# Kernel tuning notes

Measured on AMD Instinct MI355X. Metric: run time of the kernel, lower is better.

## Reference

```python
import jax, jax.numpy as jnp
import numpy as np

WIN = (2, 7, 7)  # (H, W, D) window size

def _relative_position_index(H, W, D):
    coords = np.stack(np.meshgrid(np.arange(H), np.arange(W), np.arange(D), indexing='ij'))
    cf = coords.reshape(3, -1)  # [3, N]
    rel = cf[:, :, None] - cf[:, None, :]  # [3, N, N]
    rel = rel.transpose(1, 2, 0).copy()
    rel[:, :, 0] += H - 1
    rel[:, :, 1] += W - 1
    rel[:, :, 2] += D - 1
    rel[:, :, 0] *= (2 * W - 1) * (2 * D - 1)
    rel[:, :, 1] *= 2 * D - 1
    return jnp.asarray(rel.sum(-1), dtype=jnp.int32)  # [N, N]

def setup_inputs() -> dict:
    key = jax.random.key(0)
    ks = jax.random.split(key, 7)
    H, W, D = WIN
    N = H * W * D          # 98
    C = 192
    nh = 6
    num_windows = 64
    B_ = 8 * num_windows   # 512
    x = jax.random.normal(ks[0], (B_, N, C), dtype=jnp.float32)
    # shifted-window attention mask: 0 for allowed pairs, -100 for masked
    mask = jnp.where(jax.random.uniform(ks[1], (num_windows, N, N)) < 0.9, 0.0, -100.0).astype(jnp.float32)
    qkv_w = jax.random.normal(ks[2], (3 * C, C), dtype=jnp.float32) * 0.02
    qkv_b = jnp.zeros((3 * C,), dtype=jnp.float32)
    out_w = jax.random.normal(ks[3], (C, C), dtype=jnp.float32) * 0.02
    out_b = jnp.zeros((C,), dtype=jnp.float32)
    table_len = (2 * H - 1) * (2 * W - 1) * (2 * D - 1)  # 507
    bias_table = jax.random.normal(ks[4], (table_len, nh), dtype=jnp.float32) * 0.02
    rel_index = _relative_position_index(H, W, D)
    return {"x": x, "mask": mask, "qkv_w": qkv_w, "qkv_b": qkv_b,
            "out_w": out_w, "out_b": out_b, "bias_table": bias_table,
            "rel_index": rel_index}

def reference(x, mask, qkv_w, qkv_b, out_w, out_b, bias_table, rel_index):
    B_, N, C = x.shape
    nh = bias_table.shape[1]
    d = C // nh
    scale = d ** (-0.5)
    qkv = (x @ qkv_w.T + qkv_b).reshape(B_, N, 3, nh, d)
    qkv = qkv.transpose(2, 0, 3, 1, 4)          # [3, B_, nh, N, d]
    q, k, v = qkv[0], qkv[1], qkv[2]
    attn = jnp.einsum('bhnd,bhmd->bhnm', q, k) * scale   # [B_, nh, N, N]
    bias = bias_table[rel_index]                 # [N, N, nh]
    attn = attn + bias.transpose(2, 0, 1)[None]  # add relative position bias
    nw = mask.shape[0]
    attn = attn.reshape(B_ // nw, nw, nh, N, N) + mask[None, :, None]
    attn = attn.reshape(B_, nh, N, N)
    p = jax.nn.softmax(attn, axis=-1)
    out = jnp.einsum('bhnm,bhmd->bhnd', p, v)    # [B_, nh, N, d]
    out = out.transpose(0, 2, 1, 3).reshape(B_, N, C)
    return out @ out_w.T + out_b
```

## Files before the change

### kernel.cpp

```cpp
#include <hip/hip_runtime.h>

typedef __attribute__((ext_vector_type(8))) __bf16 bf16x8;
typedef __attribute__((ext_vector_type(4))) float f32x4;
typedef __attribute__((ext_vector_type(8))) unsigned short us8;
typedef __attribute__((ext_vector_type(4))) unsigned short us4;

#define NTOK 98
#define NPAD 112
#define CDIM 192
#define NH 6
#define HD 32
#define NWIN 64
#define BWIN 512
#define MROWS (BWIN * NTOK)
#define QKVN (3 * CDIM)
#define NN (NTOK * NTOK)
#define SCALE 0.17677669529663687f

#define PREP_BIAS (NH * NN)
#define PREP_WQ (QKVN * CDIM)
#define PREP_WO (CDIM * CDIM)
#define PREP_TOT (PREP_BIAS + PREP_WQ + PREP_WO)

__device__ __forceinline__ unsigned short f2b(float f) {
  unsigned u = __builtin_bit_cast(unsigned, f);
  u += 0x7FFFu + ((u >> 16) & 1u);
  return (unsigned short)(u >> 16);
}

__device__ __forceinline__ bf16x8 ldfrag(const unsigned short* p) {
  return __builtin_bit_cast(bf16x8, *(const us8*)p);
}

__global__ __launch_bounds__(256) void k_prep(
    const float* __restrict__ table, const int* __restrict__ relidx,
    const float* __restrict__ wq, const float* __restrict__ wo,
    float* __restrict__ biasHT, unsigned short* __restrict__ wqb,
    unsigned short* __restrict__ wob) {
  int idx = blockIdx.x * 256 + threadIdx.x;
  if (idx < PREP_BIAS) {
    int h = idx / NN, ij = idx - h * NN;
    biasHT[idx] = table[relidx[ij] * NH + h];
    return;
  }
  int i2 = idx - PREP_BIAS;
  if (i2 < PREP_WQ) { if (i2 >= 0) wqb[i2] = f2b(wq[i2]); return; }
  int i3 = i2 - PREP_WQ;
  if (i3 < PREP_WO) wob[i3] = f2b(wo[i3]);
}

__global__ __launch_bounds__(256) void k_qkv(
    const float* __restrict__ x, const unsigned short* __restrict__ wqb,
    const float* __restrict__ bias, unsigned short* __restrict__ qkv) {
  __shared__ unsigned short As[128 * 200];
  __shared__ unsigned short Bs[64 * 200];
  const int tid = threadIdx.x;
  const int m0 = blockIdx.x * 128;
  for (int it = 0; it < 24; ++it) {
    int q = it * 256 + tid;
    int row = q / 48, c4 = q - row * 48;
    float4 v = *(const float4*)(x + (m0 + row) * CDIM + c4 * 4);
    us4 u = {f2b(v.x), f2b(v.y), f2b(v.z), f2b(v.w)};
    *(us4*)&As[row * 200 + c4 * 4] = u;
  }
  const int lane = tid & 63;
  const int l15 = lane & 15, hi = lane >> 4;
  const int wr = (tid >> 6) >> 1, wc = (tid >> 6) & 1;
  __syncthreads();
  for (int j = 0; j < 9; ++j) {
    for (int it = 0; it < 6; ++it) {
      int q = it * 256 + tid;
      int row = q / 24, c8 = q - row * 24;
      *(us8*)&Bs[row * 200 + c8 * 8] = *(const us8*)(wqb + (j * 64 + row) * CDIM + c8 * 8);
    }
    __syncthreads();
    f32x4 acc[4][2];
#pragma unroll
    for (int fr = 0; fr < 4; ++fr) { acc[fr][0] = (f32x4)0.f; acc[fr][1] = (f32x4)0.f; }
#pragma unroll
    for (int ks = 0; ks < 6; ++ks) {
      int k0 = ks * 32 + hi * 8;
      bf16x8 b0 = ldfrag(&Bs[(wc * 32 + l15) * 200 + k0]);
      bf16x8 b1 = ldfrag(&Bs[(wc * 32 + 16 + l15) * 200 + k0]);
#pragma unroll
      for (int fr = 0; fr < 4; ++fr) {
        bf16x8 a = ldfrag(&As[(wr * 64 + fr * 16 + l15) * 200 + k0]);
        acc[fr][0] = __builtin_amdgcn_mfma_f32_16x16x32_bf16(a, b0, acc[fr][0], 0, 0, 0);
        acc[fr][1] = __builtin_amdgcn_mfma_f32_16x16x32_bf16(a, b1, acc[fr][1], 0, 0, 0);
      }
    }
    __syncthreads();
#pragma unroll
    for (int fr = 0; fr < 4; ++fr)
#pragma unroll
      for (int fc = 0; fc < 2; ++fc) {
        int colb = j * 64 + wc * 32 + fc * 16;
        int t = (colb >= 2 * CDIM) ? 2 : (colb >= CDIM ? 1 : 0);
        int head = (colb >> 5) - t * NH;
        int d = (colb & 31) + l15;
        long pbase = ((long)(t * NH + head) * MROWS) * 32 + d;
#pragma unroll
        for (int r = 0; r < 4; ++r) {
          int row = m0 + wr * 64 + fr * 16 + hi * 4 + r;
          float v = acc[fr][fc][r] + bias[colb + l15];
          if (t == 0) v *= SCALE;
          qkv[pbase + (long)row * 32] = f2b(v);
        }
      }
  }
}

__global__ __launch_bounds__(448) void k_attn(
    const unsigned short* __restrict__ qkv, const float* __restrict__ biasHT,
    const float* __restrict__ mask, unsigned short* __restrict__ ao) {
  __shared__ unsigned short Ks[NPAD * 40];
  __shared__ unsigned short Vt[32 * 136];
  __shared__ unsigned short P[NPAD * 136];
  const int tid = threadIdx.x;
  const int h = blockIdx.x % NH;
  const int b = blockIdx.x / NH;
  const int wnd = b & (NWIN - 1);
  const int lane = tid & 63, wv = tid >> 6;
  const int l15 = lane & 15, hi = lane >> 4;
  const long rb = (long)b * NTOK;
  const unsigned short* qp = qkv + ((long)h * MROWS + rb) * 32;
  const unsigned short* kp = qkv + ((long)(NH + h) * MROWS + rb) * 32;
  const unsigned short* vp = qkv + ((long)(2 * NH + h) * MROWS + rb) * 32;
  {
    int row = tid >> 2, q = tid & 3;
    us8 kv = (us8)0;
    if (row < NTOK) kv = *(const us8*)(kp + row * 32 + q * 8);
    *(us8*)&Ks[row * 40 + q * 8] = kv;
    if (row < NTOK) {
      us8 vv = *(const us8*)(vp + row * 32 + q * 8);
#pragma unroll
      for (int i = 0; i < 8; ++i) Vt[(q * 8 + i) * 136 + row] = vv[i];
    }
    for (int i = tid; i < 32 * 38; i += 448) {
      int dd = i / 38, n = NTOK + (i - dd * 38);
      Vt[dd * 136 + n] = 0;
    }
    for (int i = tid; i < NPAD * 16; i += 448)
      P[(i >> 4) * 136 + 112 + (i & 15)] = 0;
  }
  int qn = wv * 16 + l15;
  us8 qu = (us8)0;
  if (qn < NTOK) qu = *(const us8*)(qp + qn * 32 + hi * 8);
  bf16x8 qf = __builtin_bit_cast(bf16x8, qu);
  __syncthreads();
  f32x4 sacc[7];
#pragma unroll
  for (int tc = 0; tc < 7; ++tc) {
    bf16x8 kb = ldfrag(&Ks[(tc * 16 + l15) * 40 + hi * 8]);
    sacc[tc] = __builtin_amdgcn_mfma_f32_16x16x32_bf16(qf, kb, (f32x4)0.f, 0, 0, 0);
  }
  const float* bp = biasHT + h * NN;
  const float* mp = mask + wnd * NN;
  float rsum[4];
#pragma unroll
  for (int r = 0; r < 4; ++r) {
    int row = wv * 16 + hi * 4 + r;
    float sv[7];
    float m = -1e30f;
#pragma unroll
    for (int tc = 0; tc < 7; ++tc) {
      int col = tc * 16 + l15;
      float val = -1e30f;
      if (col < NTOK && row < NTOK) {
        int o = row * NTOK + col;
        val = (sacc[tc][r] + bp[o]) + mp[o];
      }
      sv[tc] = val;
      m = fmaxf(m, val);
    }
#pragma unroll
    for (int off = 1; off < 16; off <<= 1) m = fmaxf(m, __shfl_xor(m, off));
    float s = 0.f;
#pragma unroll
    for (int tc = 0; tc < 7; ++tc) {
      float e = __expf(sv[tc] - m);
      s += e;
      P[row * 136 + tc * 16 + l15] = f2b(e);
    }
#pragma unroll
    for (int off = 1; off < 16; off <<= 1) s += __shfl_xor(s, off);
    rsum[r] = s;
  }
  f32x4 oacc[2];
  oacc[0] = (f32x4)0.f; oacc[1] = (f32x4)0.f;
#pragma unroll
  for (int ks = 0; ks < 4; ++ks) {
    int k0 = ks * 32 + hi * 8;
    bf16x8 pa = ldfrag(&P[(wv * 16 + l15) * 136 + k0]);
#pragma unroll
    for (int tc = 0; tc < 2; ++tc) {
      bf16x8 vb = ldfrag(&Vt[(tc * 16 + l15) * 136 + k0]);
      oacc[tc] = __builtin_amdgcn_mfma_f32_16x16x32_bf16(pa, vb, oacc[tc], 0, 0, 0);
    }
  }
#pragma unroll
  for (int tc = 0; tc < 2; ++tc)
#pragma unroll
    for (int r = 0; r < 4; ++r) {
      int row = wv * 16 + hi * 4 + r;
      if (row < NTOK) {
        float v = oacc[tc][r] / rsum[r];
        ao[(rb + row) * CDIM + h * HD + tc * 16 + l15] = f2b(v);
      }
    }
}

__global__ __launch_bounds__(256) void k_proj(
    const unsigned short* __restrict__ a, const unsigned short* __restrict__ wob,
    const float* __restrict__ bias, float* __restrict__ out) {
  __shared__ unsigned short As[128 * 200];
  __shared__ unsigned short Bs[64 * 200];
  const int tid = threadIdx.x;
  const int m0 = blockIdx.x * 128;
  for (int it = 0; it < 12; ++it) {
    int q = it * 256 + tid;
    int row = q / 24, c8 = q - row * 24;
    *(us8*)&As[row * 200 + c8 * 8] = *(const us8*)(a + (m0 + row) * CDIM + c8 * 8);
  }
  const int lane = tid & 63;
  const int l15 = lane & 15, hi = lane >> 4;
  const int wr = (tid >> 6) >> 1, wc = (tid >> 6) & 1;
  __syncthreads();
  for (int j = 0; j < 3; ++j) {
    for (int it = 0; it < 6; ++it) {
      int q = it * 256 + tid;
      int row = q / 24, c8 = q - row * 24;
      *(us8*)&Bs[row * 200 + c8 * 8] = *(const us8*)(wob + (j * 64 + row) * CDIM + c8 * 8);
    }
    __syncthreads();
    f32x4 acc[4][2];
#pragma unroll
    for (int fr = 0; fr < 4; ++fr) { acc[fr][0] = (f32x4)0.f; acc[fr][1] = (f32x4)0.f; }
#pragma unroll
    for (int ks = 0; ks < 6; ++ks) {
      int k0 = ks * 32 + hi * 8;
      bf16x8 b0 = ldfrag(&Bs[(wc * 32 + l15) * 200 + k0]);
      bf16x8 b1 = ldfrag(&Bs[(wc * 32 + 16 + l15) * 200 + k0]);
#pragma unroll
      for (int fr = 0; fr < 4; ++fr) {
        bf16x8 aa = ldfrag(&As[(wr * 64 + fr * 16 + l15) * 200 + k0]);
        acc[fr][0] = __builtin_amdgcn_mfma_f32_16x16x32_bf16(aa, b0, acc[fr][0], 0, 0, 0);
        acc[fr][1] = __builtin_amdgcn_mfma_f32_16x16x32_bf16(aa, b1, acc[fr][1], 0, 0, 0);
      }
    }
    __syncthreads();
#pragma unroll
    for (int fr = 0; fr < 4; ++fr)
#pragma unroll
      for (int fc = 0; fc < 2; ++fc)
#pragma unroll
        for (int r = 0; r < 4; ++r) {
          int row = m0 + wr * 64 + fr * 16 + hi * 4 + r;
          int col = j * 64 + wc * 32 + fc * 16 + l15;
          out[row * CDIM + col] = acc[fr][fc][r] + bias[col];
        }
  }
}

extern "C" void kernel_launch(void* const* d_in, const int* in_sizes, int n_in,
                              void* d_out, int out_size, void* d_ws, size_t ws_size,
                              hipStream_t stream) {
  const float* x      = (const float*)d_in[0];
  const float* mask   = (const float*)d_in[1];
  const float* qkv_w  = (const float*)d_in[2];
  const float* qkv_b  = (const float*)d_in[3];
  const float* out_w  = (const float*)d_in[4];
  const float* out_b  = (const float*)d_in[5];
  const float* table  = (const float*)d_in[6];
  const int*   relidx = (const int*)d_in[7];
  float* out = (float*)d_out;
  char* ws = (char*)d_ws;

  const size_t off_bias = 0;
  const size_t off_wqb  = 230656;
  const size_t off_wob  = 451840;
  const size_t off_qkv  = 525568;
  const size_t off_ao   = off_qkv + 57802752;
  float* biasHT = (float*)(ws + off_bias);
  unsigned short* wqb  = (unsigned short*)(ws + off_wqb);
  unsigned short* wob  = (unsigned short*)(ws + off_wob);
  unsigned short* qkvp = (unsigned short*)(ws + off_qkv);
  unsigned short* aop  = (unsigned short*)(ws + off_ao);

  k_prep<<<(PREP_TOT + 255) / 256, 256, 0, stream>>>(table, relidx, qkv_w, out_w,
                                                     biasHT, wqb, wob);
  k_qkv<<<MROWS / 128, 256, 0, stream>>>(x, wqb, qkv_b, qkvp);
  k_attn<<<BWIN * NH, 448, 0, stream>>>(qkvp, biasHT, mask, aop);
  k_proj<<<MROWS / 128, 256, 0, stream>>>(aop, wob, out_b, out);
}
```

Baseline: 198.2 us.

## Fuse QKV projection and attention per window, premerge bias and mask

Replaces the separate QKV GEMM and attention kernels with one kernel per window. It computes Q, K and V for all six heads into LDS and then runs attention for each head. This removes the global write and re-read of the full bf16 QKV tensor. The prep kernel now builds one combined relative-position-bias-plus-mask table per window and head, so attention does a single load per score instead of two. The cost is a large LDS footprint that allows only one 448-thread block per CU. The weight tiles are also restaged nine times per block with barriers, and the merged table adds about 15 MB of prep writes per call.

```diff
diff --git a/kernel.cpp b/kernel.cpp
--- a/kernel.cpp
+++ b/kernel.cpp
@@ -6,21 +6,24 @@
 typedef __attribute__((ext_vector_type(4))) unsigned short us4;
 
 #define NTOK 98
-#define NPAD 112
 #define CDIM 192
 #define NH 6
-#define HD 32
 #define NWIN 64
 #define BWIN 512
 #define MROWS (BWIN * NTOK)
-#define QKVN (3 * CDIM)
 #define NN (NTOK * NTOK)
 #define SCALE 0.17677669529663687f
 
-#define PREP_BIAS (NH * NN)
-#define PREP_WQ (QKVN * CDIM)
+#define PREP_BM (NWIN * NH * NN)
+#define PREP_WQ (3 * CDIM * CDIM)
 #define PREP_WO (CDIM * CDIM)
-#define PREP_TOT (PREP_BIAS + PREP_WQ + PREP_WO)
+#define PREP_TOT (PREP_BM + PREP_WQ + PREP_WO)
+
+#define OFF_AS 0
+#define OFF_W  39200
+#define OFF_K  64800
+#define OFF_VT 118560
+#define LDS_TOT 161824
 
 __device__ __forceinline__ unsigned short f2b(float f) {
   unsigned u = __builtin_bit_cast(unsigned, f);
@@ -34,180 +37,197 @@
 
 __global__ __launch_bounds__(256) void k_prep(
     const float* __restrict__ table, const int* __restrict__ relidx,
-    const float* __restrict__ wq, const float* __restrict__ wo,
-    float* __restrict__ biasHT, unsigned short* __restrict__ wqb,
-    unsigned short* __restrict__ wob) {
+    const float* __restrict__ mask, const float* __restrict__ wq,
+    const float* __restrict__ wo, float* __restrict__ bm,
+    unsigned short* __restrict__ wqb, unsigned short* __restrict__ wob) {
   int idx = blockIdx.x * 256 + threadIdx.x;
-  if (idx < PREP_BIAS) {
-    int h = idx / NN, ij = idx - h * NN;
-    biasHT[idx] = table[relidx[ij] * NH + h];
+  if (idx < PREP_BM) {
+    int w = idx / (NH * NN);
+    int r = idx - w * NH * NN;
+    int h = r / NN, ij = r - h * NN;
+    bm[idx] = table[relidx[ij] * NH + h] + mask[w * NN + ij];
     return;
   }
-  int i2 = idx - PREP_BIAS;
-  if (i2 < PREP_WQ) { if (i2 >= 0) wqb[i2] = f2b(wq[i2]); return; }
+  int i2 = idx - PREP_BM;
+  if (i2 < PREP_WQ) { wqb[i2] = f2b(wq[i2]); return; }
   int i3 = i2 - PREP_WQ;
-  if (i3 < PREP_WO) wob[i3] = f2b(wo[i3]);
-}
-
-__global__ __launch_bounds__(256) void k_qkv(
+  if (i3 < PREP_TOT - PREP_BM - PREP_WQ) wob[i3] = f2b(wo[i3]);
+}
+
+__global__ __launch_bounds__(448, 2) void k_fused(
     const float* __restrict__ x, const unsigned short* __restrict__ wqb,
-    const float* __restrict__ bias, unsigned short* __restrict__ qkv) {
-  __shared__ unsigned short As[128 * 200];
-  __shared__ unsigned short Bs[64 * 200];
+    const float* __restrict__ qkv_b, const float* __restrict__ bm,
+    unsigned short* __restrict__ ao) {
+  extern __shared__ char smem[];
+  unsigned short* As = (unsigned short*)(smem + OFF_AS);
+  unsigned short* Ws = (unsigned short*)(smem + OFF_W);
+  unsigned short* Ks = (unsigned short*)(smem + OFF_K);
+  unsigned short* Vt = (unsigned short*)(smem + OFF_VT);
   const int tid = threadIdx.x;
-  const int m0 = blockIdx.x * 128;
-  for (int it = 0; it < 24; ++it) {
-    int q = it * 256 + tid;
-    int row = q / 48, c4 = q - row * 48;
-    float4 v = *(const float4*)(x + (m0 + row) * CDIM + c4 * 4);
-    us4 u = {f2b(v.x), f2b(v.y), f2b(v.z), f2b(v.w)};
-    *(us4*)&As[row * 200 + c4 * 4] = u;
-  }
-  const int lane = tid & 63;
-  const int l15 = lane & 15, hi = lane >> 4;
-  const int wr = (tid >> 6) >> 1, wc = (tid >> 6) & 1;
-  __syncthreads();
-  for (int j = 0; j < 9; ++j) {
-    for (int it = 0; it < 6; ++it) {
-      int q = it * 256 + tid;
-      int row = q / 24, c8 = q - row * 24;
-      *(us8*)&Bs[row * 200 + c8 * 8] = *(const us8*)(wqb + (j * 64 + row) * CDIM + c8 * 8);
-    }
-    __syncthreads();
-    f32x4 acc[4][2];
-#pragma unroll
-    for (int fr = 0; fr < 4; ++fr) { acc[fr][0] = (f32x4)0.f; acc[fr][1] = (f32x4)0.f; }
-#pragma unroll
-    for (int ks = 0; ks < 6; ++ks) {
-      int k0 = ks * 32 + hi * 8;
-      bf16x8 b0 = ldfrag(&Bs[(wc * 32 + l15) * 200 + k0]);
-      bf16x8 b1 = ldfrag(&Bs[(wc * 32 + 16 + l15) * 200 + k0]);
-#pragma unroll
-      for (int fr = 0; fr < 4; ++fr) {
-        bf16x8 a = ldfrag(&As[(wr * 64 + fr * 16 + l15) * 200 + k0]);
-        acc[fr][0] = __builtin_amdgcn_mfma_f32_16x16x32_bf16(a, b0, acc[fr][0], 0, 0, 0);
-        acc[fr][1] = __builtin_amdgcn_mfma_f32_16x16x32_bf16(a, b1, acc[fr][1], 0, 0, 0);
-      }
-    }
-    __syncthreads();
-#pragma unroll
-    for (int fr = 0; fr < 4; ++fr)
-#pragma unroll
-      for (int fc = 0; fc < 2; ++fc) {
-        int colb = j * 64 + wc * 32 + fc * 16;
-        int t = (colb >= 2 * CDIM) ? 2 : (colb >= CDIM ? 1 : 0);
-        int head = (colb >> 5) - t * NH;
-        int d = (colb & 31) + l15;
-        long pbase = ((long)(t * NH + head) * MROWS) * 32 + d;
-#pragma unroll
-        for (int r = 0; r < 4; ++r) {
-          int row = m0 + wr * 64 + fr * 16 + hi * 4 + r;
-          float v = acc[fr][fc][r] + bias[colb + l15];
-          if (t == 0) v *= SCALE;
-          qkv[pbase + (long)row * 32] = f2b(v);
-        }
-      }
-  }
-}
-
-__global__ __launch_bounds__(448) void k_attn(
-    const unsigned short* __restrict__ qkv, const float* __restrict__ biasHT,
-    const float* __restrict__ mask, unsigned short* __restrict__ ao) {
-  __shared__ unsigned short Ks[NPAD * 40];
-  __shared__ unsigned short Vt[32 * 136];
-  __shared__ unsigned short P[NPAD * 136];
-  const int tid = threadIdx.x;
-  const int h = blockIdx.x % NH;
-  const int b = blockIdx.x / NH;
-  const int wnd = b & (NWIN - 1);
+  const int b = blockIdx.x;
   const int lane = tid & 63, wv = tid >> 6;
   const int l15 = lane & 15, hi = lane >> 4;
-  const long rb = (long)b * NTOK;
-  const unsigned short* qp = qkv + ((long)h * MROWS + rb) * 32;
-  const unsigned short* kp = qkv + ((long)(NH + h) * MROWS + rb) * 32;
-  const unsigned short* vp = qkv + ((long)(2 * NH + h) * MROWS + rb) * 32;
-  {
-    int row = tid >> 2, q = tid & 3;
-    us8 kv = (us8)0;
-    if (row < NTOK) kv = *(const us8*)(kp + row * 32 + q * 8);
-    *(us8*)&Ks[row * 40 + q * 8] = kv;
-    if (row < NTOK) {
-      us8 vv = *(const us8*)(vp + row * 32 + q * 8);
-#pragma unroll
-      for (int i = 0; i < 8; ++i) Vt[(q * 8 + i) * 136 + row] = vv[i];
-    }
-    for (int i = tid; i < 32 * 38; i += 448) {
-      int dd = i / 38, n = NTOK + (i - dd * 38);
-      Vt[dd * 136 + n] = 0;
-    }
-    for (int i = tid; i < NPAD * 16; i += 448)
-      P[(i >> 4) * 136 + 112 + (i & 15)] = 0;
-  }
-  int qn = wv * 16 + l15;
-  us8 qu = (us8)0;
-  if (qn < NTOK) qu = *(const us8*)(qp + qn * 32 + hi * 8);
-  bf16x8 qf = __builtin_bit_cast(bf16x8, qu);
+  unsigned short* scr = Ws + wv * 640;
+
+  for (int it = 0; it < 11; ++it) {
+    int q = it * 448 + tid;
+    if (q < 98 * 48) {
+      int row = q / 48, c4 = q - row * 48;
+      float4 v = *(const float4*)(x + ((size_t)b * NTOK + row) * CDIM + c4 * 4);
+      us4 u = {f2b(v.x), f2b(v.y), f2b(v.z), f2b(v.w)};
+      *(us4*)&As[row * 200 + c4 * 4] = u;
+    }
+  }
+
+#define STAGEW(J)                                                              \
+  for (int it = 0; it < 4; ++it) {                                             \
+    int q = it * 448 + tid;                                                    \
+    if (q < 1536) {                                                            \
+      int row = q / 24, c8 = q - row * 24;                                     \
+      *(us8*)&Ws[row * 200 + c8 * 8] =                                         \
+          *(const us8*)(wqb + ((J) * 64 + row) * CDIM + c8 * 8);               \
+    }                                                                          \
+  }
+
+#define DOMFMA(ACC)                                                            \
+  _Pragma("unroll") for (int ks = 0; ks < 6; ++ks) {                           \
+    int k0 = ks * 32 + hi * 8;                                                 \
+    bf16x8 a = ldfrag(&As[(wv * 16 + l15) * 200 + k0]);                        \
+    _Pragma("unroll") for (int fc = 0; fc < 4; ++fc) {                         \
+      bf16x8 bw = ldfrag(&Ws[(fc * 16 + l15) * 200 + k0]);                     \
+      ACC[fc] = __builtin_amdgcn_mfma_f32_16x16x32_bf16(a, bw, ACC[fc], 0, 0, 0); \
+    }                                                                          \
+  }
+
+  bf16x8 qregs[6];
+#pragma unroll
+  for (int j = 0; j < 3; ++j) {
+    __syncthreads();
+    STAGEW(j);
+    __syncthreads();
+    f32x4 acc[4];
+#pragma unroll
+    for (int fc = 0; fc < 4; ++fc) acc[fc] = (f32x4)0.f;
+    DOMFMA(acc);
+    __syncthreads();
+#pragma unroll
+    for (int hh = 0; hh < 2; ++hh) {
+#pragma unroll
+      for (int fc2 = 0; fc2 < 2; ++fc2) {
+        int fc = hh * 2 + fc2;
+        float bia = qkv_b[j * 64 + fc * 16 + l15];
+#pragma unroll
+        for (int r = 0; r < 4; ++r)
+          scr[(hi * 4 + r) * 40 + fc2 * 16 + l15] = f2b((acc[fc][r] + bia) * SCALE);
+      }
+      qregs[2 * j + hh] = ldfrag(&scr[l15 * 40 + hi * 8]);
+    }
+  }
+  for (int j = 3; j < 9; ++j) {
+    __syncthreads();
+    STAGEW(j);
+    __syncthreads();
+    f32x4 acc[4];
+#pragma unroll
+    for (int fc = 0; fc < 4; ++fc) acc[fc] = (f32x4)0.f;
+    DOMFMA(acc);
+    __syncthreads();
+    if (j < 6) {
+#pragma unroll
+      for (int fc = 0; fc < 4; ++fc) {
+        int c = j * 64 + fc * 16 + l15;
+        int ci = c - CDIM, head = ci >> 5, d = ci & 31;
+        float bia = qkv_b[c];
+#pragma unroll
+        for (int r = 0; r < 4; ++r)
+          Ks[head * 4480 + (wv * 16 + hi * 4 + r) * 40 + d] = f2b(acc[fc][r] + bia);
+      }
+    } else {
+#pragma unroll
+      for (int fc = 0; fc < 4; ++fc) {
+        int c = j * 64 + fc * 16 + l15;
+        int ci = c - 2 * CDIM, head = ci >> 5, d = ci & 31;
+        float bia = qkv_b[c];
+        us4 u = {f2b(acc[fc][0] + bia), f2b(acc[fc][1] + bia),
+                 f2b(acc[fc][2] + bia), f2b(acc[fc][3] + bia)};
+        *(us4*)&Vt[head * 3584 + d * 112 + wv * 16 + hi * 4] = u;
+      }
+    }
+  }
   __syncthreads();
-  f32x4 sacc[7];
-#pragma unroll
-  for (int tc = 0; tc < 7; ++tc) {
-    bf16x8 kb = ldfrag(&Ks[(tc * 16 + l15) * 40 + hi * 8]);
-    sacc[tc] = __builtin_amdgcn_mfma_f32_16x16x32_bf16(qf, kb, (f32x4)0.f, 0, 0, 0);
-  }
-  const float* bp = biasHT + h * NN;
-  const float* mp = mask + wnd * NN;
-  float rsum[4];
-#pragma unroll
-  for (int r = 0; r < 4; ++r) {
-    int row = wv * 16 + hi * 4 + r;
-    float sv[7];
-    float m = -1e30f;
+  for (int i = tid; i < NH * 32 * 16; i += 448) {
+    int hd = i >> 4, tk = 98 + (i & 15);
+    if (tk < 112) Vt[hd * 112 + tk] = 0;
+  }
+  if (tid < 64) *(unsigned*)((char*)Vt + 43008 + tid * 4) = 0u;
+  unsigned short* Pw = As + wv * 2176;
+  *(us4*)&Pw[(lane >> 2) * 136 + 112 + (lane & 3) * 4] = (us4)(unsigned short)0;
+  __syncthreads();
+
+  const int wnd = b & (NWIN - 1);
+#pragma unroll
+  for (int h = 0; h < NH; ++h) {
+    const unsigned short* Kh = Ks + h * 4480;
+    const unsigned short* Vh = Vt + h * 3584;
+    bf16x8 qf = qregs[h];
+    f32x4 sacc[7];
 #pragma unroll
     for (int tc = 0; tc < 7; ++tc) {
-      int col = tc * 16 + l15;
-      float val = -1e30f;
-      if (col < NTOK && row < NTOK) {
-        int o = row * NTOK + col;
-        val = (sacc[tc][r] + bp[o]) + mp[o];
-      }
-      sv[tc] = val;
-      m = fmaxf(m, val);
-    }
-#pragma unroll
-    for (int off = 1; off < 16; off <<= 1) m = fmaxf(m, __shfl_xor(m, off));
-    float s = 0.f;
-#pragma unroll
-    for (int tc = 0; tc < 7; ++tc) {
-      float e = __expf(sv[tc] - m);
-      s += e;
-      P[row * 136 + tc * 16 + l15] = f2b(e);
-    }
-#pragma unroll
-    for (int off = 1; off < 16; off <<= 1) s += __shfl_xor(s, off);
-    rsum[r] = s;
-  }
-  f32x4 oacc[2];
-  oacc[0] = (f32x4)0.f; oacc[1] = (f32x4)0.f;
-#pragma unroll
-  for (int ks = 0; ks < 4; ++ks) {
-    int k0 = ks * 32 + hi * 8;
-    bf16x8 pa = ldfrag(&P[(wv * 16 + l15) * 136 + k0]);
-#pragma unroll
-    for (int tc = 0; tc < 2; ++tc) {
-      bf16x8 vb = ldfrag(&Vt[(tc * 16 + l15) * 136 + k0]);
-      oacc[tc] = __builtin_amdgcn_mfma_f32_16x16x32_bf16(pa, vb, oacc[tc], 0, 0, 0);
-    }
-  }
-#pragma unroll
-  for (int tc = 0; tc < 2; ++tc)
+      bf16x8 kb = ldfrag(&Kh[(tc * 16 + l15) * 40 + hi * 8]);
+      sacc[tc] = __builtin_amdgcn_mfma_f32_16x16x32_bf16(qf, kb, (f32x4)0.f, 0, 0, 0);
+    }
+    const float* bmp = bm + (size_t)(wnd * NH + h) * NN;
+    float rsum[4];
 #pragma unroll
     for (int r = 0; r < 4; ++r) {
       int row = wv * 16 + hi * 4 + r;
-      if (row < NTOK) {
-        float v = oacc[tc][r] / rsum[r];
-        ao[(rb + row) * CDIM + h * HD + tc * 16 + l15] = f2b(v);
-      }
-    }
+      float sv[7];
+      float m = -1e30f;
+#pragma unroll
+      for (int tc = 0; tc < 7; ++tc) {
+        int col = tc * 16 + l15;
+        float val = -1e30f;
+        if (col < NTOK && row < NTOK) val = sacc[tc][r] + bmp[row * NTOK + col];
+        sv[tc] = val;
+        m = fmaxf(m, val);
+      }
+#pragma unroll
+      for (int off = 1; off < 16; off <<= 1) m = fmaxf(m, __shfl_xor(m, off));
+      float s = 0.f;
+#pragma unroll
+      for (int tc = 0; tc < 7; ++tc) {
+        float e = __expf(sv[tc] - m);
+        s += e;
+        Pw[(hi * 4 + r) * 136 + tc * 16 + l15] = f2b(e);
+      }
+#pragma unroll
+      for (int off = 1; off < 16; off <<= 1) s += __shfl_xor(s, off);
+      rsum[r] = s;
+    }
+    f32x4 oacc[2];
+    oacc[0] = (f32x4)0.f; oacc[1] = (f32x4)0.f;
+#pragma unroll
+    for (int ks = 0; ks < 4; ++ks) {
+      int k0 = ks * 32 + hi * 8;
+      bf16x8 pa = ldfrag(&Pw[l15 * 136 + k0]);
+#pragma unroll
+      for (int tc2 = 0; tc2 < 2; ++tc2) {
+        bf16x8 vb = ldfrag(&Vh[(tc2 * 16 + l15) * 112 + k0]);
+        oacc[tc2] = __builtin_amdgcn_mfma_f32_16x16x32_bf16(pa, vb, oacc[tc2], 0, 0, 0);
+      }
+    }
+#pragma unroll
+    for (int tc2 = 0; tc2 < 2; ++tc2)
+#pragma unroll
+      for (int r = 0; r < 4; ++r) {
+        int row = wv * 16 + hi * 4 + r;
+        if (row < NTOK)
+          ao[((size_t)b * NTOK + row) * CDIM + h * 32 + tc2 * 16 + l15] =
+              f2b(oacc[tc2][r] / rsum[r]);
+      }
+  }
+#undef STAGEW
+#undef DOMFMA
 }
 
 __global__ __launch_bounds__(256) void k_proj(
@@ -276,20 +296,18 @@
   float* out = (float*)d_out;
   char* ws = (char*)d_ws;
 
-  const size_t off_bias = 0;
-  const size_t off_wqb  = 230656;
-  const size_t off_wob  = 451840;
-  const size_t off_qkv  = 525568;
-  const size_t off_ao   = off_qkv + 57802752;
-  float* biasHT = (float*)(ws + off_bias);
-  unsigned short* wqb  = (unsigned short*)(ws + off_wqb);
-  unsigned short* wob  = (unsigned short*)(ws + off_wob);
-  unsigned short* qkvp = (unsigned short*)(ws + off_qkv);
-  unsigned short* aop  = (unsigned short*)(ws + off_ao);
-
-  k_prep<<<(PREP_TOT + 255) / 256, 256, 0, stream>>>(table, relidx, qkv_w, out_w,
-                                                     biasHT, wqb, wob);
-  k_qkv<<<MROWS / 128, 256, 0, stream>>>(x, wqb, qkv_b, qkvp);
-  k_attn<<<BWIN * NH, 448, 0, stream>>>(qkvp, biasHT, mask, aop);
+  float* bm            = (float*)ws;
+  unsigned short* wqb  = (unsigned short*)(ws + 14751744);
+  unsigned short* wob  = (unsigned short*)(ws + 14972928);
+  unsigned short* aop  = (unsigned short*)(ws + 15046656);
+
+  static int lds_set = 0;
+  (void)lds_set;
+  hipFuncSetAttribute((const void*)k_fused,
+                      hipFuncAttributeMaxDynamicSharedMemorySize, LDS_TOT);
+
+  k_prep<<<(PREP_TOT + 255) / 256, 256, 0, stream>>>(table, relidx, mask, qkv_w,
+                                                     out_w, bm, wqb, wob);
+  k_fused<<<BWIN, 448, LDS_TOT, stream>>>(x, wqb, qkv_b, bm, aop);
   k_proj<<<MROWS / 128, 256, 0, stream>>>(aop, wob, out_b, out);
 }
```

After: 268.9 us. 35.6% more time.

## Premerge bias and mask per window, read K from global, convert out_w inline

Applied to the files above, without the earlier changes.

The prep kernel now writes one combined relative-position-bias-plus-mask tensor per window and head, so the attention kernel does one load per score instead of two. The attention kernel no longer stages K in shared memory: it reads K fragments straight from global with clamped row indices, uses clamped unconditional loads for bias/mask, and adds an occupancy hint to launch bounds. The projection kernel converts fp32 out_w to bf16 on the fly instead of relying on a pre-converted copy. The bf16 qkv weights are placed in the attention-output buffer to save workspace. The trade-off is a larger prep pass and a bigger per-window bias tensor (64x6x98x98 floats) streamed through memory.

```diff
diff --git a/kernel.cpp b/kernel.cpp
--- a/kernel.cpp
+++ b/kernel.cpp
@@ -6,21 +6,17 @@
 typedef __attribute__((ext_vector_type(4))) unsigned short us4;
 
 #define NTOK 98
-#define NPAD 112
 #define CDIM 192
 #define NH 6
-#define HD 32
 #define NWIN 64
 #define BWIN 512
 #define MROWS (BWIN * NTOK)
-#define QKVN (3 * CDIM)
 #define NN (NTOK * NTOK)
 #define SCALE 0.17677669529663687f
 
-#define PREP_BIAS (NH * NN)
-#define PREP_WQ (QKVN * CDIM)
-#define PREP_WO (CDIM * CDIM)
-#define PREP_TOT (PREP_BIAS + PREP_WQ + PREP_WO)
+#define PREP_BM (NWIN * NH * NN)
+#define PREP_WQ (3 * CDIM * CDIM)
+#define PREP_TOT (PREP_BM + PREP_WQ)
 
 __device__ __forceinline__ unsigned short f2b(float f) {
   unsigned u = __builtin_bit_cast(unsigned, f);
@@ -34,19 +30,18 @@
 
 __global__ __launch_bounds__(256) void k_prep(
     const float* __restrict__ table, const int* __restrict__ relidx,
-    const float* __restrict__ wq, const float* __restrict__ wo,
-    float* __restrict__ biasHT, unsigned short* __restrict__ wqb,
-    unsigned short* __restrict__ wob) {
+    const float* __restrict__ mask, const float* __restrict__ wq,
+    float* __restrict__ bm, unsigned short* __restrict__ wqb) {
   int idx = blockIdx.x * 256 + threadIdx.x;
-  if (idx < PREP_BIAS) {
-    int h = idx / NN, ij = idx - h * NN;
-    biasHT[idx] = table[relidx[ij] * NH + h];
+  if (idx < PREP_BM) {
+    int w = idx / (NH * NN);
+    int r = idx - w * NH * NN;
+    int h = r / NN, ij = r - h * NN;
+    bm[idx] = table[relidx[ij] * NH + h] + mask[w * NN + ij];
     return;
   }
-  int i2 = idx - PREP_BIAS;
-  if (i2 < PREP_WQ) { if (i2 >= 0) wqb[i2] = f2b(wq[i2]); return; }
-  int i3 = i2 - PREP_WQ;
-  if (i3 < PREP_WO) wob[i3] = f2b(wo[i3]);
+  int i2 = idx - PREP_BM;
+  if (i2 < PREP_WQ) wqb[i2] = f2b(wq[i2]);
 }
 
 __global__ __launch_bounds__(256) void k_qkv(
@@ -110,12 +105,11 @@
   }
 }
 
-__global__ __launch_bounds__(448) void k_attn(
-    const unsigned short* __restrict__ qkv, const float* __restrict__ biasHT,
-    const float* __restrict__ mask, unsigned short* __restrict__ ao) {
-  __shared__ unsigned short Ks[NPAD * 40];
+__global__ __launch_bounds__(448, 6) void k_attn(
+    const unsigned short* __restrict__ qkv, const float* __restrict__ bm,
+    unsigned short* __restrict__ ao) {
   __shared__ unsigned short Vt[32 * 136];
-  __shared__ unsigned short P[NPAD * 136];
+  __shared__ unsigned short P[112 * 136];
   const int tid = threadIdx.x;
   const int h = blockIdx.x % NH;
   const int b = blockIdx.x / NH;
@@ -128,9 +122,6 @@
   const unsigned short* vp = qkv + ((long)(2 * NH + h) * MROWS + rb) * 32;
   {
     int row = tid >> 2, q = tid & 3;
-    us8 kv = (us8)0;
-    if (row < NTOK) kv = *(const us8*)(kp + row * 32 + q * 8);
-    *(us8*)&Ks[row * 40 + q * 8] = kv;
     if (row < NTOK) {
       us8 vv = *(const us8*)(vp + row * 32 + q * 8);
 #pragma unroll
@@ -140,7 +131,7 @@
       int dd = i / 38, n = NTOK + (i - dd * 38);
       Vt[dd * 136 + n] = 0;
     }
-    for (int i = tid; i < NPAD * 16; i += 448)
+    for (int i = tid; i < 112 * 16; i += 448)
       P[(i >> 4) * 136 + 112 + (i & 15)] = 0;
   }
   int qn = wv * 16 + l15;
@@ -151,25 +142,25 @@
   f32x4 sacc[7];
 #pragma unroll
   for (int tc = 0; tc < 7; ++tc) {
-    bf16x8 kb = ldfrag(&Ks[(tc * 16 + l15) * 40 + hi * 8]);
+    int rowc = tc * 16 + l15;
+    rowc = rowc > 97 ? 97 : rowc;
+    bf16x8 kb = ldfrag(kp + rowc * 32 + hi * 8);
     sacc[tc] = __builtin_amdgcn_mfma_f32_16x16x32_bf16(qf, kb, (f32x4)0.f, 0, 0, 0);
   }
-  const float* bp = biasHT + h * NN;
-  const float* mp = mask + wnd * NN;
+  const float* bmp = bm + (size_t)(wnd * NH + h) * NN;
   float rsum[4];
 #pragma unroll
   for (int r = 0; r < 4; ++r) {
     int row = wv * 16 + hi * 4 + r;
+    int rowc = row > 97 ? 97 : row;
     float sv[7];
     float m = -1e30f;
 #pragma unroll
     for (int tc = 0; tc < 7; ++tc) {
       int col = tc * 16 + l15;
-      float val = -1e30f;
-      if (col < NTOK && row < NTOK) {
-        int o = row * NTOK + col;
-        val = (sacc[tc][r] + bp[o]) + mp[o];
-      }
+      int colc = col > 97 ? 97 : col;
+      float bmv = bmp[rowc * NTOK + colc];
+      float val = (col < NTOK && row < NTOK) ? sacc[tc][r] + bmv : -1e30f;
       sv[tc] = val;
       m = fmaxf(m, val);
     }
@@ -193,25 +184,25 @@
     int k0 = ks * 32 + hi * 8;
     bf16x8 pa = ldfrag(&P[(wv * 16 + l15) * 136 + k0]);
 #pragma unroll
-    for (int tc = 0; tc < 2; ++tc) {
-      bf16x8 vb = ldfrag(&Vt[(tc * 16 + l15) * 136 + k0]);
-      oacc[tc] = __builtin_amdgcn_mfma_f32_16x16x32_bf16(pa, vb, oacc[tc], 0, 0, 0);
-    }
-  }
-#pragma unroll
-  for (int tc = 0; tc < 2; ++tc)
+    for (int tc2 = 0; tc2 < 2; ++tc2) {
+      bf16x8 vb = ldfrag(&Vt[(tc2 * 16 + l15) * 136 + k0]);
+      oacc[tc2] = __builtin_amdgcn_mfma_f32_16x16x32_bf16(pa, vb, oacc[tc2], 0, 0, 0);
+    }
+  }
+#pragma unroll
+  for (int tc2 = 0; tc2 < 2; ++tc2)
 #pragma unroll
     for (int r = 0; r < 4; ++r) {
       int row = wv * 16 + hi * 4 + r;
       if (row < NTOK) {
-        float v = oacc[tc][r] / rsum[r];
-        ao[(rb + row) * CDIM + h * HD + tc * 16 + l15] = f2b(v);
+        float v = oacc[tc2][r] / rsum[r];
+        ao[(rb + row) * CDIM + h * 32 + tc2 * 16 + l15] = f2b(v);
       }
     }
 }
 
 __global__ __launch_bounds__(256) void k_proj(
-    const unsigned short* __restrict__ a, const unsigned short* __restrict__ wob,
+    const unsigned short* __restrict__ a, const float* __restrict__ w,
     const float* __restrict__ bias, float* __restrict__ out) {
   __shared__ unsigned short As[128 * 200];
   __shared__ unsigned short Bs[64 * 200];
@@ -227,10 +218,12 @@
   const int wr = (tid >> 6) >> 1, wc = (tid >> 6) & 1;
   __syncthreads();
   for (int j = 0; j < 3; ++j) {
-    for (int it = 0; it < 6; ++it) {
+    for (int it = 0; it < 12; ++it) {
       int q = it * 256 + tid;
-      int row = q / 24, c8 = q - row * 24;
-      *(us8*)&Bs[row * 200 + c8 * 8] = *(const us8*)(wob + (j * 64 + row) * CDIM + c8 * 8);
+      int row = q / 48, c4 = q - row * 48;
+      float4 v = *(const float4*)(w + (j * 64 + row) * CDIM + c4 * 4);
+      us4 u = {f2b(v.x), f2b(v.y), f2b(v.z), f2b(v.w)};
+      *(us4*)&Bs[row * 200 + c4 * 4] = u;
     }
     __syncthreads();
     f32x4 acc[4][2];
@@ -276,20 +269,13 @@
   float* out = (float*)d_out;
   char* ws = (char*)d_ws;
 
-  const size_t off_bias = 0;
-  const size_t off_wqb  = 230656;
-  const size_t off_wob  = 451840;
-  const size_t off_qkv  = 525568;
-  const size_t off_ao   = off_qkv + 57802752;
-  float* biasHT = (float*)(ws + off_bias);
-  unsigned short* wqb  = (unsigned short*)(ws + off_wqb);
-  unsigned short* wob  = (unsigned short*)(ws + off_wob);
-  unsigned short* qkvp = (unsigned short*)(ws + off_qkv);
-  unsigned short* aop  = (unsigned short*)(ws + off_ao);
-
-  k_prep<<<(PREP_TOT + 255) / 256, 256, 0, stream>>>(table, relidx, qkv_w, out_w,
-                                                     biasHT, wqb, wob);
+  float* bm            = (float*)ws;
+  unsigned short* qkvp = (unsigned short*)(ws + 14751744);
+  unsigned short* aop  = (unsigned short*)(ws + 72554496);
+  unsigned short* wqb  = aop;
+
+  k_prep<<<PREP_TOT / 256, 256, 0, stream>>>(table, relidx, mask, qkv_w, bm, wqb);
   k_qkv<<<MROWS / 128, 256, 0, stream>>>(x, wqb, qkv_b, qkvp);
-  k_attn<<<BWIN * NH, 448, 0, stream>>>(qkvp, biasHT, mask, aop);
-  k_proj<<<MROWS / 128, 256, 0, stream>>>(aop, wob, out_b, out);
-}
+  k_attn<<<BWIN * NH, 448, 0, stream>>>(qkvp, bm, aop);
+  k_proj<<<MROWS / 128, 256, 0, stream>>>(aop, out_w, out_b, out);
+}
```

After: 208.9 us. 1.05x slower.
